# Kernel tuning notes

Measured on AMD Instinct MI355X. Metric: run time of the kernel, lower is better.

Reference implementation:

```python
import jax, jax.numpy as jnp
import numpy as np

# fixed 9 neighborhood offsets (center + 8 directions), in pixel units
BASE = np.array([[0,0],[-1,-1],[0,-1],[1,-1],[-1,0],[1,0],[-1,1],[0,1],[1,1]], dtype=np.float32)
MAX_DELTA = 0.5 / 512.0


def bilinear_sample(vm, gx, gy):
    """vm: (D,H,W); gx,gy: (N,) normalized grid coords in [-1,1].
    Bilinear, padding_mode='zeros', align_corners=True. Returns (D,N)."""
    D, H, W = vm.shape
    ix = (gx + 1.0) * 0.5 * (W - 1)
    iy = (gy + 1.0) * 0.5 * (H - 1)
    x0 = jnp.floor(ix); y0 = jnp.floor(iy)
    x1 = x0 + 1.0;      y1 = y0 + 1.0
    wx1 = ix - x0; wx0 = 1.0 - wx1
    wy1 = iy - y0; wy0 = 1.0 - wy1
    fm = vm.reshape(D, H * W)

    def corner(xf, yf, wx, wy):
        valid = (xf >= 0) & (xf <= W - 1) & (yf >= 0) & (yf <= H - 1)
        xi = jnp.clip(xf.astype(jnp.int32), 0, W - 1)
        yi = jnp.clip(yf.astype(jnp.int32), 0, H - 1)
        v = jnp.take(fm, yi * W + xi, axis=1)  # (D,N) gather
        w = jnp.where(valid, wx * wy, 0.0)
        return v * w

    return (corner(x0, y0, wx0, wy0) + corner(x1, y0, wx1, wy0)
            + corner(x0, y1, wx0, wy1) + corner(x1, y1, wx1, wy1))


def setup_inputs() -> dict:
    key = jax.random.key(0)
    ks = jax.random.split(key, 5)
    B, C, Hf, Wf = 4, 256, 128, 128
    T, D = 16384, 128
    fmap = jax.random.normal(ks[0], (B, C, Hf, Wf), dtype=jnp.float32)
    coords = jax.random.uniform(ks[1], (B, T, 2), dtype=jnp.float32)
    W_proj = jax.random.normal(ks[2], (D, C), dtype=jnp.float32) * (1.0 / np.sqrt(C))
    W1 = jax.random.normal(ks[3], (D, D), dtype=jnp.float32) * (1.0 / np.sqrt(D))
    b1 = jnp.zeros((D,), dtype=jnp.float32)
    W2 = jax.random.normal(ks[4], (2, D), dtype=jnp.float32) * (1.0 / np.sqrt(D))
    b2 = jnp.zeros((2,), dtype=jnp.float32)
    return {"fmap": fmap, "coords": coords, "W_proj": W_proj,
            "W1": W1, "b1": b1, "W2": W2, "b2": b2}


def reference(fmap, coords, W_proj, W1, b1, W2, b2):
    B, C, Hf, Wf = fmap.shape
    T = coords.shape[1]
    K = BASE.shape[0]
    # 1x1 conv projection
    vm = jnp.einsum('bchw,dc->bdhw', fmap, W_proj)  # (B,D,Hf,Wf)
    # offsets: one pixel step in [0,1] coords (align_corners=True)
    step = jnp.array([1.0 / (Wf - 1), 1.0 / (Hf - 1)], dtype=coords.dtype)
    grid = coords[:, :, None, :] + jnp.asarray(BASE)[None, None] * step  # (B,T,K,2)
    grid = grid * 2.0 - 1.0                                            # normalize to [-1,1]
    grid = grid.reshape(B, T * K, 2)
    feat = jax.vmap(bilinear_sample)(vm, grid[..., 0], grid[..., 1])   # (B,D,T*K)
    D = feat.shape[1]
    feat = feat.transpose(0, 2, 1).reshape(B, T, K, D).mean(axis=2)    # (B,T,D)
    h = jax.nn.relu(feat @ W1.T + b1)
    delta = jnp.tanh(h @ W2.T + b2) * MAX_DELTA
    return coords + delta
```

## Files before the change

### kernel.cpp

```cpp
#include <hip/hip_runtime.h>
#include <cstddef>

#define NB 4
#define NC 256
#define ND 128
#define NH 128
#define NW 128
#define NHW (NH*NW)
#define NT 16384
#define NBKT 1024
#define CAP 192
#define FS 136

typedef short   short8  __attribute__((ext_vector_type(8)));
typedef unsigned short ushort8 __attribute__((ext_vector_type(8)));
typedef float   floatx4 __attribute__((ext_vector_type(4)));
typedef float   floatx2 __attribute__((ext_vector_type(2)));

__device__ __forceinline__ unsigned pk_bf16(float a, float b) {
    unsigned ua = __float_as_uint(a);
    unsigned ub = __float_as_uint(b);
    ua += 0x7fffu + ((ua >> 16) & 1u);
    ub += 0x7fffu + ((ub >> 16) & 1u);
    return (ua >> 16) | (ub & 0xffff0000u);
}

__device__ __forceinline__ unsigned fp8x4_from_f32(float v0, float v1, float v2, float v3) {
    int r = 0;
    r = __builtin_amdgcn_cvt_pk_fp8_f32(v0, v1, r, false);
    r = __builtin_amdgcn_cvt_pk_fp8_f32(v2, v3, r, true);
    return (unsigned)r;
}
template <bool HI>
__device__ __forceinline__ floatx2 fp8x2_to_f32(unsigned w) {
    return __builtin_amdgcn_cvt_pk_f32_fp8((int)w, HI);
}

__device__ __forceinline__ int bucket_of(float cx, float cy, int b) {
    int x0 = (int)floorf(cx * (float)(NW - 1));
    int y0 = (int)floorf(cy * (float)(NH - 1));
    x0 = min(max(x0, 0), NW - 1);
    y0 = min(max(y0, 0), NH - 1);
    return b * 256 + (y0 >> 3) * 16 + (x0 >> 3);
}

__global__ __launch_bounds__(1024)
void fill_kernel(const float* __restrict__ coords, const float* __restrict__ W1,
                 int* __restrict__ counts, int* __restrict__ order,
                 unsigned short* __restrict__ W1bf)
{
    const int bi = blockIdx.x;
    if (bi >= 64) {
        const int i = (bi - 64) * 1024 + threadIdx.x;
        unsigned u = __float_as_uint(W1[i]);
        u += 0x7fffu + ((u >> 16) & 1u);
        W1bf[i] = (unsigned short)(u >> 16);
        return;
    }
    const int g = bi * 1024 + threadIdx.x;
    const float cx = coords[(size_t)g*2 + 0];
    const float cy = coords[(size_t)g*2 + 1];
    const int bkt = bucket_of(cx, cy, g >> 14);
    const int pos = atomicAdd(&counts[bkt], 1);
    if (pos < CAP) order[bkt*CAP + pos] = g;
}

__global__ __launch_bounds__(512, 4)
void proj_kernel(const float* __restrict__ fmap, const float* __restrict__ Wp,
                 unsigned char* __restrict__ vm)
{
    const int bi = blockIdx.x;
    __shared__ unsigned short awp[8*8*64*8];

    const int t    = threadIdx.x;
    const int lane = t & 63;
    const int w    = t >> 6;
    const int l15  = lane & 15;
    const int q    = lane >> 4;
    const int cq   = q * 8;

    {
        const int dt = w;
        const float* wr0 = Wp + (size_t)(dt*16 + l15)*NC + cq;
        #pragma unroll
        for (int ch = 0; ch < 8; ++ch) {
            float4 g0 = *(const float4*)(wr0 + ch*32);
            float4 g1 = *(const float4*)(wr0 + ch*32 + 4);
            uint4 pk = make_uint4(pk_bf16(g0.x,g0.y), pk_bf16(g0.z,g0.w),
                                  pk_bf16(g1.x,g1.y), pk_bf16(g1.z,g1.w));
            *(uint4*)&awp[((dt*8 + ch)*64 + lane)*8] = pk;
        }
    }
    __syncthreads();

    const int b    = (bi & 7) >> 1;
    const int slot = ((bi >> 3) << 1) | (bi & 1);
    const int p    = slot*128 + w*16 + l15;

    floatx4 acc[8];
    #pragma unroll
    for (int i = 0; i < 8; ++i) acc[i] = (floatx4)(0.f);

    const float* fbase = fmap + (size_t)b*NC*NHW + p;

    #pragma unroll
    for (int c0 = 0; c0 < 8; ++c0) {
        const float* bp = fbase + (size_t)(c0*32 + cq)*NHW;
        float f[8];
        #pragma unroll
        for (int j = 0; j < 8; ++j) f[j] = bp[(size_t)j*NHW];
        union { short8 v; unsigned u[4]; } bc;
        #pragma unroll
        for (int j = 0; j < 4; ++j) bc.u[j] = pk_bf16(f[2*j], f[2*j+1]);
        #pragma unroll
        for (int dt = 0; dt < 8; ++dt) {
            short8 afr = *(const short8*)&awp[((dt*8 + c0)*64 + lane)*8];
            acc[dt] = __builtin_amdgcn_mfma_f32_16x16x32_bf16(afr, bc.v, acc[dt], 0, 0, 0);
        }
    }
    unsigned char* vrow = vm + ((size_t)(b*NHW + p))*ND;
    #pragma unroll
    for (int dt = 0; dt < 8; ++dt) {
        floatx4 v = acc[dt];
        *(unsigned*)&vrow[dt*16 + q*4] = fp8x4_from_f32(v[0], v[1], v[2], v[3]);
    }
}

__global__ __launch_bounds__(512, 4)
void gather_mlp(const unsigned char* __restrict__ vm, const float* __restrict__ coords,
                const int* __restrict__ counts, const int* __restrict__ order,
                const unsigned short* __restrict__ W1bf, const float* __restrict__ b1,
                const float* __restrict__ W2, const float* __restrict__ b2,
                float* __restrict__ out)
{
    __shared__ unsigned short feat[64 * FS];
    __shared__ float part[64][8];
    __shared__ float W2s[256];
    __shared__ float b1s[128];
    __shared__ int gidx[64];
    const int t   = threadIdx.x;
    const int bkt = blockIdx.x;
    const int n      = min(counts[bkt], CAP);
    const int chunks = (n + 63) >> 6;

    if (t < 128) {
        W2s[t*2]   = W2[t];
        W2s[t*2+1] = W2[ND + t];
        b1s[t]     = b1[t];
    }
    __syncthreads();

    for (int c = 0; c < chunks; ++c) {
        const int np = min(n - c*64, 64);

        {
            const int pt = t >> 3;
            const int c8 = t & 7;
            if (pt < np) {
                const int g = order[bkt*CAP + c*64 + pt];
                if (c8 == 0) gidx[pt] = g;
                const int b = g >> 14;
                const float cx = coords[(size_t)g*2 + 0];
                const float cy = coords[(size_t)g*2 + 1];
                const float ix = cx * (float)(NW - 1);
                const float iy = cy * (float)(NH - 1);
                const float x0f = floorf(ix), y0f = floorf(iy);
                const int x0 = (int)x0f, y0 = (int)y0f;
                const float wx1 = ix - x0f, wy1 = iy - y0f;
                const float wxv[4] = {1.f - wx1, 1.f, 1.f, wx1};
                const float wyv[4] = {1.f - wy1, 1.f, 1.f, wy1};
                floatx2 acc[8];
                #pragma unroll
                for (int k = 0; k < 8; ++k) acc[k] = (floatx2)(0.f);
                const unsigned char* vmb = vm + (size_t)b*NHW*ND + c8*16;
                #pragma unroll
                for (int j = 0; j < 4; ++j) {
                    const int Y  = y0 - 1 + j;
                    const int Yc = min(max(Y, 0), NH-1);
                    const bool vy = (Y >= 0) & (Y < NH);
                    #pragma unroll
                    for (int i = 0; i < 4; ++i) {
                        const int X  = x0 - 1 + i;
                        const int Xc = min(max(X, 0), NW-1);
                        const bool vx = (X >= 0) & (X < NW);
                        const float wgt = (vx & vy) ? wxv[i]*wyv[j] : 0.f;
                        uint4 u = *(const uint4*)(vmb + (size_t)(Yc*NW + Xc)*ND);
                        const floatx2 w2 = {wgt, wgt};
                        acc[0] += w2 * fp8x2_to_f32<false>(u.x);
                        acc[1] += w2 * fp8x2_to_f32<true >(u.x);
                        acc[2] += w2 * fp8x2_to_f32<false>(u.y);
                        acc[3] += w2 * fp8x2_to_f32<true >(u.y);
                        acc[4] += w2 * fp8x2_to_f32<false>(u.z);
                        acc[5] += w2 * fp8x2_to_f32<true >(u.z);
                        acc[6] += w2 * fp8x2_to_f32<false>(u.w);
                        acc[7] += w2 * fp8x2_to_f32<true >(u.w);
                    }
                }
                const float s9 = 1.f/9.f;
                unsigned pk[8];
                #pragma unroll
                for (int k = 0; k < 8; ++k)
                    pk[k] = pk_bf16(acc[k].x*s9, acc[k].y*s9);
                *(uint4*)&feat[pt*FS + c8*16]     = make_uint4(pk[0],pk[1],pk[2],pk[3]);
                *(uint4*)&feat[pt*FS + c8*16 + 8] = make_uint4(pk[4],pk[5],pk[6],pk[7]);
            }
        }
        __syncthreads();

        {
            const int lane = t & 63;
            const int w    = t >> 6;
            const int l15  = lane & 15;
            const int q    = lane >> 4;
            const int mp   = w & 3;
            const int npr  = w >> 2;

            floatx4 C[2][2];
            #pragma unroll
            for (int mi = 0; mi < 2; ++mi)
                #pragma unroll
                for (int ni = 0; ni < 2; ++ni) C[mi][ni] = (floatx4)(0.f);

            #pragma unroll
            for (int kk = 0; kk < 4; ++kk) {
                short8 a0 = *(const short8*)&W1bf[((mp*2+0)*16 + l15)*ND + kk*32 + q*8];
                short8 a1 = *(const short8*)&W1bf[((mp*2+1)*16 + l15)*ND + kk*32 + q*8];
                short8 f0 = *(const short8*)&feat[((npr*2+0)*16 + l15)*FS + kk*32 + q*8];
                short8 f1 = *(const short8*)&feat[((npr*2+1)*16 + l15)*FS + kk*32 + q*8];
                C[0][0] = __builtin_amdgcn_mfma_f32_16x16x32_bf16(a0, f0, C[0][0], 0, 0, 0);
                C[0][1] = __builtin_amdgcn_mfma_f32_16x16x32_bf16(a0, f1, C[0][1], 0, 0, 0);
                C[1][0] = __builtin_amdgcn_mfma_f32_16x16x32_bf16(a1, f0, C[1][0], 0, 0, 0);
                C[1][1] = __builtin_amdgcn_mfma_f32_16x16x32_bf16(a1, f1, C[1][1], 0, 0, 0);
            }
            #pragma unroll
            for (int ni = 0; ni < 2; ++ni) {
                float s0 = 0.f, s1 = 0.f;
                #pragma unroll
                for (int mi = 0; mi < 2; ++mi) {
                    const int e0 = (mp*2 + mi)*16 + q*4;
                    float4 bq = *(const float4*)&b1s[e0];
                    floatx4 h4 = C[mi][ni];
                    #pragma unroll
                    for (int r = 0; r < 4; ++r) {
                        float hv = fmaxf(h4[r] + (&bq.x)[r], 0.f);
                        float2 wv = *(const float2*)&W2s[(e0 + r)*2];
                        s0 = fmaf(hv, wv.x, s0);
                        s1 = fmaf(hv, wv.y, s1);
                    }
                }
                s0 += __shfl_xor(s0, 16); s0 += __shfl_xor(s0, 32);
                s1 += __shfl_xor(s1, 16); s1 += __shfl_xor(s1, 32);
                if (q == 0) {
                    const int pt = (npr*2 + ni)*16 + l15;
                    part[pt][mp*2 + 0] = s0;
                    part[pt][mp*2 + 1] = s1;
                }
            }
        }
        __syncthreads();

        if (t < np) {
            const int g = gidx[t];
            float s0 = part[t][0] + part[t][2] + part[t][4] + part[t][6];
            float s1 = part[t][1] + part[t][3] + part[t][5] + part[t][7];
            const float cx = coords[(size_t)g*2 + 0];
            const float cy = coords[(size_t)g*2 + 1];
            const float MD = 0.5f / 512.0f;
            float2 o = make_float2(cx + tanhf(s0 + b2[0]) * MD,
                                   cy + tanhf(s1 + b2[1]) * MD);
            *(float2*)&out[(size_t)g*2] = o;
        }
        __syncthreads();
    }
}

extern "C" void kernel_launch(void* const* d_in, const int* in_sizes, int n_in,
                              void* d_out, int out_size, void* d_ws, size_t ws_size,
                              hipStream_t stream)
{
    const float* fmap   = (const float*)d_in[0];
    const float* coords = (const float*)d_in[1];
    const float* Wp     = (const float*)d_in[2];
    const float* W1     = (const float*)d_in[3];
    const float* b1     = (const float*)d_in[4];
    const float* W2     = (const float*)d_in[5];
    const float* b2     = (const float*)d_in[6];
    float* out = (float*)d_out;

    unsigned char* vm = (unsigned char*)d_ws;
    char* base = (char*)d_ws + (size_t)NB*NHW*ND;
    unsigned short* W1bf = (unsigned short*)base;
    int* counts = (int*)(base + 32768);
    int* order  = (int*)(base + 32768 + 4096);

    hipMemsetAsync(counts, 0, NBKT*sizeof(int), stream);
    fill_kernel<<<dim3(64 + 16), 1024, 0, stream>>>(coords, W1, counts, order, W1bf);
    proj_kernel<<<dim3(512),      512, 0, stream>>>(fmap, Wp, vm);
    gather_mlp <<<dim3(NBKT),     512, 0, stream>>>(vm, coords, counts, order,
                                                    W1bf, b1, W2, b2, out);
}
```

Baseline: 152.0 us.

## Fuse fill into projection kernel and split projection output across two blocks

Merges the bucket-fill and W1 conversion work into the projection kernel launch, removing one kernel launch and its boundary. The projection is split so each block computes half of the 128 output channels, doubling the block count and halving accumulators and shared memory per block. The split makes two blocks read the same fmap pixels, relying on cache reuse between adjacent blocks to avoid doubling DRAM traffic.

```diff
diff --git a/kernel.cpp b/kernel.cpp
--- a/kernel.cpp
+++ b/kernel.cpp
@@ -44,33 +44,32 @@
     return b * 256 + (y0 >> 3) * 16 + (x0 >> 3);
 }
 
-__global__ __launch_bounds__(1024)
-void fill_kernel(const float* __restrict__ coords, const float* __restrict__ W1,
-                 int* __restrict__ counts, int* __restrict__ order,
-                 unsigned short* __restrict__ W1bf)
+__global__ __launch_bounds__(512, 4)
+void proj_fill_kernel(const float* __restrict__ fmap, const float* __restrict__ Wp,
+                      const float* __restrict__ coords, const float* __restrict__ W1,
+                      unsigned char* __restrict__ vm,
+                      int* __restrict__ counts, int* __restrict__ order,
+                      unsigned short* __restrict__ W1bf)
 {
-    const int bi = blockIdx.x;
-    if (bi >= 64) {
-        const int i = (bi - 64) * 1024 + threadIdx.x;
+    const int bi0 = blockIdx.x;
+    if (bi0 < 128) {
+        const int g = bi0 * 512 + threadIdx.x;
+        const float cx = coords[(size_t)g*2 + 0];
+        const float cy = coords[(size_t)g*2 + 1];
+        const int bkt = bucket_of(cx, cy, g >> 14);
+        const int pos = atomicAdd(&counts[bkt], 1);
+        if (pos < CAP) order[bkt*CAP + pos] = g;
+        return;
+    }
+    if (bi0 < 160) {
+        const int i = (bi0 - 128) * 512 + threadIdx.x;
         unsigned u = __float_as_uint(W1[i]);
         u += 0x7fffu + ((u >> 16) & 1u);
         W1bf[i] = (unsigned short)(u >> 16);
         return;
     }
-    const int g = bi * 1024 + threadIdx.x;
-    const float cx = coords[(size_t)g*2 + 0];
-    const float cy = coords[(size_t)g*2 + 1];
-    const int bkt = bucket_of(cx, cy, g >> 14);
-    const int pos = atomicAdd(&counts[bkt], 1);
-    if (pos < CAP) order[bkt*CAP + pos] = g;
-}
-
-__global__ __launch_bounds__(512, 4)
-void proj_kernel(const float* __restrict__ fmap, const float* __restrict__ Wp,
-                 unsigned char* __restrict__ vm)
-{
-    const int bi = blockIdx.x;
-    __shared__ unsigned short awp[8*8*64*8];
+    const int bi = bi0 - 160;
+    __shared__ unsigned short awp[4*8*64*8];
 
     const int t    = threadIdx.x;
     const int lane = t & 63;
@@ -79,11 +78,19 @@
     const int q    = lane >> 4;
     const int cq   = q * 8;
 
+    const int h    = bi & 1;
+    const int bi2  = bi >> 1;
+    const int b    = (bi2 & 7) >> 1;
+    const int slot = ((bi2 >> 3) << 1) | (bi2 & 1);
+    const int p    = slot*128 + w*16 + l15;
+
     {
-        const int dt = w;
-        const float* wr0 = Wp + (size_t)(dt*16 + l15)*NC + cq;
+        const int dt  = w >> 1;
+        const int ch0 = (w & 1) * 4;
+        const float* wr0 = Wp + (size_t)(h*64 + dt*16 + l15)*NC + cq;
         #pragma unroll
-        for (int ch = 0; ch < 8; ++ch) {
+        for (int cc = 0; cc < 4; ++cc) {
+            const int ch = ch0 + cc;
             float4 g0 = *(const float4*)(wr0 + ch*32);
             float4 g1 = *(const float4*)(wr0 + ch*32 + 4);
             uint4 pk = make_uint4(pk_bf16(g0.x,g0.y), pk_bf16(g0.z,g0.w),
@@ -93,13 +100,9 @@
     }
     __syncthreads();
 
-    const int b    = (bi & 7) >> 1;
-    const int slot = ((bi >> 3) << 1) | (bi & 1);
-    const int p    = slot*128 + w*16 + l15;
-
-    floatx4 acc[8];
+    floatx4 acc[4];
     #pragma unroll
-    for (int i = 0; i < 8; ++i) acc[i] = (floatx4)(0.f);
+    for (int i = 0; i < 4; ++i) acc[i] = (floatx4)(0.f);
 
     const float* fbase = fmap + (size_t)b*NC*NHW + p;
 
@@ -113,14 +116,14 @@
         #pragma unroll
         for (int j = 0; j < 4; ++j) bc.u[j] = pk_bf16(f[2*j], f[2*j+1]);
         #pragma unroll
-        for (int dt = 0; dt < 8; ++dt) {
+        for (int dt = 0; dt < 4; ++dt) {
             short8 afr = *(const short8*)&awp[((dt*8 + c0)*64 + lane)*8];
             acc[dt] = __builtin_amdgcn_mfma_f32_16x16x32_bf16(afr, bc.v, acc[dt], 0, 0, 0);
         }
     }
-    unsigned char* vrow = vm + ((size_t)(b*NHW + p))*ND;
+    unsigned char* vrow = vm + ((size_t)(b*NHW + p))*ND + h*64;
     #pragma unroll
-    for (int dt = 0; dt < 8; ++dt) {
+    for (int dt = 0; dt < 4; ++dt) {
         floatx4 v = acc[dt];
         *(unsigned*)&vrow[dt*16 + q*4] = fp8x4_from_f32(v[0], v[1], v[2], v[3]);
     }
@@ -294,8 +297,8 @@
     int* order  = (int*)(base + 32768 + 4096);
 
     hipMemsetAsync(counts, 0, NBKT*sizeof(int), stream);
-    fill_kernel<<<dim3(64 + 16), 1024, 0, stream>>>(coords, W1, counts, order, W1bf);
-    proj_kernel<<<dim3(512),      512, 0, stream>>>(fmap, Wp, vm);
-    gather_mlp <<<dim3(NBKT),     512, 0, stream>>>(vm, coords, counts, order,
-                                                    W1bf, b1, W2, b2, out);
-}
+    proj_fill_kernel<<<dim3(160 + 1024), 512, 0, stream>>>(
+        fmap, Wp, coords, W1, vm, counts, order, W1bf);
+    gather_mlp<<<dim3(NBKT), 512, 0, stream>>>(vm, coords, counts, order,
+                                               W1bf, b1, W2, b2, out);
+}
```

Result: slower. 159.1 us (+4.7%).
